# Optimization experiments

Hardware: AMD Instinct MI355X
Metric: run time of the kernel (lower is better)

The kernel has to match this reference:

```python
import jax, jax.numpy as jnp
import numpy as np

EPS = 1e-5
NEG = 0.1  # LeakyReLU slope


def _conv(x, w, stride=1, pad=0):
    return jax.lax.conv_general_dilated(
        x, w, (stride, stride), [(pad, pad), (pad, pad)],
        dimension_numbers=('NCHW', 'OIHW', 'NCHW'))


def _bn(x, p):
    # p: [4, C] stacked (gamma, beta, running_mean, running_var); eval-mode BN
    g, b, m, v = p[0], p[1], p[2], p[3]
    inv = g / jnp.sqrt(v + EPS)
    return x * inv[None, :, None, None] + (b - m * inv)[None, :, None, None]


def _lrelu(x):
    return jnp.where(x >= 0, x, NEG * x)


def _mdcn(x, w_off, b_off, w_dcn, b_dcn, G=2, K=3, pad=1):
    # ModulatedDeformConvPack (DCNv2): conv_offset -> (dy, dx, mask), then
    # modulated bilinear sampling + dense contraction with the conv weight.
    B, C, H, W = x.shape
    K2 = K * K
    off = _conv(x, w_off, 1, pad) + b_off[None, :, None, None]  # [B, 3*G*K2, H, W]
    dy, dx, ml = jnp.split(off, 3, axis=1)
    dy = dy.reshape(B, G, K2, H, W)
    dx = dx.reshape(B, G, K2, H, W)
    mask = jax.nn.sigmoid(ml).reshape(B, G, K2, H, W)
    kyv, kxv = np.meshgrid(np.arange(K), np.arange(K), indexing='ij')
    ky = jnp.asarray(kyv.reshape(K2), x.dtype)
    kx = jnp.asarray(kxv.reshape(K2), x.dtype)
    ii = jnp.arange(H, dtype=x.dtype)
    jj = jnp.arange(W, dtype=x.dtype)
    # sample coords: p0 + p_k + offset (stride 1, dilation 1)
    py = ii[None, None, None, :, None] - pad + ky[None, None, :, None, None] + dy
    px = jj[None, None, None, None, :] - pad + kx[None, None, :, None, None] + dx
    Cg = C // G
    # [B, G, H*W, Cg] layout so the bilinear gather indexes a small int tensor
    imgs = x.reshape(B, G, Cg, H, W).transpose(0, 1, 3, 4, 2).reshape(B, G, H * W, Cg)
    y0 = jnp.floor(py)
    x0 = jnp.floor(px)
    N = K2 * H * W
    wy = (py - y0).reshape(B, G, N, 1)
    wx = (px - x0).reshape(B, G, N, 1)

    def gather(yi, xi):
        valid = (yi >= 0) & (yi <= H - 1) & (xi >= 0) & (xi <= W - 1)
        yc = jnp.clip(yi, 0, H - 1).astype(jnp.int32)
        xc = jnp.clip(xi, 0, W - 1).astype(jnp.int32)
        idx = (yc * W + xc).reshape(B, G, N, 1)
        v = jnp.take_along_axis(imgs, idx, axis=2)  # [B, G, N, Cg]
        return v * valid.reshape(B, G, N, 1).astype(x.dtype)

    v00 = gather(y0, x0)
    v01 = gather(y0, x0 + 1)
    v10 = gather(y0 + 1, x0)
    v11 = gather(y0 + 1, x0 + 1)
    val = (v00 * (1 - wy) * (1 - wx) + v01 * (1 - wy) * wx
           + v10 * wy * (1 - wx) + v11 * wy * wx)
    val = (val * mask.reshape(B, G, N, 1)).reshape(B, G, K2, H, W, Cg)
    wr = w_dcn.reshape(w_dcn.shape[0], G, Cg, K2)
    out = jnp.einsum('bgkijc,ogck->boij', val, wr)
    return out + b_dcn[None, :, None, None]


def _forward(x, w_r1, bn_r1, w_r2, bn_r2, w_rs, bn_rs, w_off, b_off,
             w_dcn, b_dcn, bn1, w_c2, bn2, w_ds, bn_ds):
    # ResBlock(in=64, out=128, stride=2): conv3x3/s2-BN-LReLU-conv3x3-BN + 1x1/s2 shortcut
    h = _lrelu(_bn(_conv(x, w_r1, 2, 1), bn_r1))
    h = _bn(_conv(h, w_r2, 1, 1), bn_r2)
    sc = _bn(_conv(x, w_rs, 2, 0), bn_rs)
    h = _lrelu(h + sc)
    # modulated deformable conv 3x3, deformable_groups=2
    h = _lrelu(_bn(_mdcn(h, w_off, b_off, w_dcn, b_dcn), bn1))
    h = _lrelu(_bn(_conv(h, w_c2, 1, 0), bn2))
    # DeconBlock residual (downsample since in!=out, stride!=1)
    res = _bn(_conv(x, w_ds, 2, 0), bn_ds)
    return res + h


def setup_inputs() -> dict:
    key = jax.random.key(0)
    ks = jax.random.split(key, 16)
    f32 = jnp.float32

    def n(k, shape, s):
        return jax.random.normal(k, shape, f32) * s

    def bnp(k, c):
        # gamma, beta, mean, var — var kept >= 0.1 for stability
        return jax.random.uniform(k, (4, c), f32, 0.1, 1.0)

    return {
        'x': n(ks[0], (4, 64, 192, 192), 1.0),
        'w_r1': n(ks[1], (128, 64, 3, 3), 0.04),
        'bn_r1': bnp(ks[2], 128),
        'w_r2': n(ks[3], (128, 128, 3, 3), 0.03),
        'bn_r2': bnp(ks[4], 128),
        'w_rs': n(ks[5], (128, 64, 1, 1), 0.12),
        'bn_rs': bnp(ks[6], 128),
        'w_off': n(ks[7], (54, 128, 3, 3), 0.01),  # small => offsets of a few px
        'b_off': n(ks[8], (54,), 0.1),
        'w_dcn': n(ks[9], (128, 128, 3, 3), 0.03),
        'b_dcn': n(ks[10], (128,), 0.1),
        'bn1': bnp(ks[11], 128),
        'w_c2': n(ks[12], (128, 128, 1, 1), 0.09),
        'bn2': bnp(ks[13], 128),
        'w_ds': n(ks[14], (128, 64, 1, 1), 0.12),
        'bn_ds': bnp(ks[15], 128),
    }


def reference(x, w_r1, bn_r1, w_r2, bn_r2, w_rs, bn_rs, w_off, b_off,
              w_dcn, b_dcn, bn1, w_c2, bn2, w_ds, bn_ds):
    return _forward(x, w_r1, bn_r1, w_r2, bn_r2, w_rs, bn_rs, w_off, b_off,
                    w_dcn, b_dcn, bn1, w_c2, bn2, w_ds, bn_ds)
```

## Files before the change

### kernel.cpp

```cpp
#include <hip/hip_runtime.h>
#include <hip/hip_bf16.h>
#include <cstdint>

#define EPS 1e-5f
#define NEG 0.1f

using bfrag = __attribute__((ext_vector_type(8))) short;
using f32x4 = __attribute__((ext_vector_type(4))) float;
typedef unsigned short ushort_t;

constexpr int B_  = 4,  CIN = 64, H0 = 192, W0 = 192;
constexpr int C_  = 128, H_ = 96, W_ = 96;
constexpr int HW_ = H_ * W_;
constexpr int HW0 = H0 * W0;
constexpr int XS  = 194;
constexpr int TS  = 98;
constexpr int VSTR = 1160;

__device__ __forceinline__ ushort_t f2bf(float f) {
  unsigned u = __builtin_bit_cast(unsigned, f);
  u += 0x7fffu + ((u >> 16) & 1u);
  return (ushort_t)(u >> 16);
}
__device__ __forceinline__ float loF(unsigned d) {
  return __builtin_bit_cast(float, d << 16);
}
__device__ __forceinline__ float hiF(unsigned d) {
  return __builtin_bit_cast(float, d & 0xFFFF0000u);
}
__device__ __forceinline__ bfrag loadB(const ushort_t* p) {
  return *(const bfrag*)p;
}

#define MFMA4(A0, A1, B0, B1, ACC)                                             \
  ACC[0][0] = __builtin_amdgcn_mfma_f32_16x16x32_bf16(A0, B0, ACC[0][0], 0, 0, 0); \
  ACC[0][1] = __builtin_amdgcn_mfma_f32_16x16x32_bf16(A0, B1, ACC[0][1], 0, 0, 0); \
  ACC[1][0] = __builtin_amdgcn_mfma_f32_16x16x32_bf16(A1, B0, ACC[1][0], 0, 0, 0); \
  ACC[1][1] = __builtin_amdgcn_mfma_f32_16x16x32_bf16(A1, B1, ACC[1][1], 0, 0, 0);

__global__ __launch_bounds__(256)
void k_prep(const float* __restrict__ w_r1, const float* __restrict__ w_r2,
            const float* __restrict__ w_off, const float* __restrict__ w_dcn,
            const float* __restrict__ w_rs, const float* __restrict__ w_c2,
            const float* __restrict__ w_ds,
            ushort_t* __restrict__ wp_r1, ushort_t* __restrict__ wp_r2,
            ushort_t* __restrict__ wp_off, ushort_t* __restrict__ wp_dcn,
            ushort_t* __restrict__ wp_rs, ushort_t* __restrict__ wp_c2,
            ushort_t* __restrict__ wp_ds,
            ushort_t* __restrict__ xclp, ushort_t* __restrict__ t1p,
            ushort_t* __restrict__ t3p) {
  int bi = blockIdx.x;
  int tid = (int)threadIdx.x;
  auto pack3w = [&](const float* w, ushort_t* wp, int O, int C, int Opad, int b0) {
    int idx = (bi - b0) * 256 + tid;
    int e = idx & 7;
    int lane = (idx >> 3) & 63;
    int fb = idx >> 9;
    int OBQ = Opad / 16;
    int obq = fb % OBQ, s = fb / OBQ;
    int lr = lane & 15, lq = lane >> 4;
    int o = obq * 16 + lr;
    int cq = s % (C / 32), tap = s / (C / 32);
    int c = cq * 32 + lq * 8 + e;
    wp[idx] = (o < O) ? f2bf(w[((size_t)o * C + c) * 9 + tap]) : (ushort_t)0;
  };
  auto pack1w = [&](const float* w, ushort_t* wp, int O, int C, int Opad, int b0) {
    int idx = (bi - b0) * 256 + tid;
    int e = idx & 7;
    int lane = (idx >> 3) & 63;
    int fb = idx >> 9;
    int OBQ = Opad / 16;
    int obq = fb % OBQ, s = fb / OBQ;
    int lr = lane & 15, lq = lane >> 4;
    int o = obq * 16 + lr;
    int c = s * 32 + lq * 8 + e;
    wp[idx] = (o < O) ? f2bf(w[(size_t)o * C + c]) : (ushort_t)0;
  };
  auto border = [&](ushort_t* buf, int N, int C, int b0) {
    int idx = (bi - b0) * 256 + tid;
    int per = 4 * N - 4;
    if (idx >= per * 4) return;
    int b = idx / per, e = idx - b * per;
    int r, s;
    if (e < N) { r = 0; s = e; }
    else if (e < 2 * N) { r = N - 1; s = e - N; }
    else if (e < 3 * N - 2) { r = e - 2 * N + 1; s = 0; }
    else { r = e - (3 * N - 2) + 1; s = N - 1; }
    uint4* p = (uint4*)(buf + ((size_t)(b * N + r) * N + s) * C);
#pragma unroll
    for (int t = 0; t < 16; ++t) { if (t < C / 8) p[t] = make_uint4(0, 0, 0, 0); }
  };
  if      (bi <  288) pack3w(w_r1,  wp_r1, 128,  64, 128, 0);
  else if (bi <  864) pack3w(w_r2,  wp_r2, 128, 128, 128, 288);
  else if (bi < 1152) pack3w(w_off, wp_off, 54, 128,  64, 864);
  else if (bi < 1728) pack3w(w_dcn, wp_dcn, 128, 128, 128, 1152);
  else if (bi < 1760) pack1w(w_rs,  wp_rs, 128,  64, 128, 1728);
  else if (bi < 1824) pack1w(w_c2,  wp_c2, 128, 128, 128, 1760);
  else if (bi < 1856) pack1w(w_ds,  wp_ds, 128,  64, 128, 1824);
  else if (bi < 1869) border(xclp, XS, 64, 1856);
  else if (bi < 1876) border(t1p, TS, 128, 1869);
  else                border(t3p, TS, 128, 1876);
}

__global__ __launch_bounds__(256)
void k_xcl(const float* __restrict__ x, ushort_t* __restrict__ xclp) {
  __shared__ float tile[64][65];
  int tx = threadIdx.x, ty = threadIdx.y;
  int cx = blockIdx.x, y = blockIdx.y, b = blockIdx.z;
  const float* src = x + (size_t)b * CIN * HW0 + (size_t)y * W0 + cx * 64;
#pragma unroll
  for (int r = 0; r < 16; ++r) {
    int ch = r * 4 + ty;
    tile[ch][tx] = src[(size_t)ch * HW0 + tx];
  }
  __syncthreads();
  ushort_t* dst = xclp + ((size_t)(b * XS + y + 1) * XS + cx * 64 + 1) * 64;
#pragma unroll
  for (int r = 0; r < 16; ++r) {
    int pp = r * 4 + ty;
    dst[(size_t)pp * 64 + tx] = f2bf(tile[tx][pp]);
  }
}

__global__ __launch_bounds__(256)
void k_conv1(const ushort_t* __restrict__ xclp, const ushort_t* __restrict__ wp,
             const float* __restrict__ bnp, ushort_t* __restrict__ t1p) {
  __shared__ ushort_t at[3 * 66 * 64];
  int tid = threadIdx.x, lane = tid & 63, wv = tid >> 6;
  int lr = lane & 15, lq = lane >> 4, ob = wv * 32;
  int j0 = blockIdx.x * 32, i = blockIdx.y, b = blockIdx.z;
  for (int t = tid; t < 1584; t += 256) {
    int ky = t / 528, r = t - ky * 528;
    int p = r >> 3, c8 = r & 7;
    const char* src = (const char*)(xclp +
        ((size_t)(b * XS + 2 * i + ky) * XS + 2 * j0) * 64) + p * 128 + c8 * 16;
    int db = ((ky * 66 + p) * 128 + c8 * 16) ^ (((p >> 1) & 7) << 4);
    *(uint4*)((char*)at + db) = *(const uint4*)src;
  }
  __syncthreads();
  f32x4 acc[2][2] = {};
#pragma unroll
  for (int tap = 0; tap < 9; ++tap) {
    int ky = tap / 3, kx = tap - 3 * ky;
    int pxa = 2 * lr + kx, pxb = 2 * (16 + lr) + kx;
#pragma unroll
    for (int cq = 0; cq < 2; ++cq) {
      bfrag a0 = *(const bfrag*)((const char*)at +
          (((ky * 66 + pxa) * 128 + cq * 64 + lq * 16) ^ (((pxa >> 1) & 7) << 4)));
      bfrag a1 = *(const bfrag*)((const char*)at +
          (((ky * 66 + pxb) * 128 + cq * 64 + lq * 16) ^ (((pxb >> 1) & 7) << 4)));
      int s = tap * 2 + cq;
      bfrag b0 = loadB(wp + (size_t)(s * 8 + wv * 2) * 512 + lane * 8);
      bfrag b1 = loadB(wp + (size_t)(s * 8 + wv * 2 + 1) * 512 + lane * 8);
      MFMA4(a0, a1, b0, b1, acc);
    }
  }
  ushort_t* dst = t1p + ((size_t)(b * TS + i + 1) * TS + j0 + 1) * 128;
#pragma unroll
  for (int nf = 0; nf < 2; ++nf) {
    int o = ob + nf * 16 + lr;
    float inv = bnp[o] * rsqrtf(bnp[384 + o] + EPS);
    float bb = bnp[128 + o] - bnp[256 + o] * inv;
#pragma unroll
    for (int mf = 0; mf < 2; ++mf)
#pragma unroll
      for (int jj = 0; jj < 4; ++jj) {
        int pix = mf * 16 + 4 * lq + jj;
        float r = acc[mf][nf][jj] * inv + bb;
        r = r >= 0.f ? r : NEG * r;
        dst[(size_t)pix * 128 + o] = f2bf(r);
      }
  }
}

__global__ __launch_bounds__(256)
void k_conv2(const ushort_t* __restrict__ t1p, const ushort_t* __restrict__ xclp,
             const ushort_t* __restrict__ wp2, const ushort_t* __restrict__ wprs,
             const float* __restrict__ bn2p, const float* __restrict__ bnsp,
             ushort_t* __restrict__ t3p) {
  __shared__ ushort_t at[3 * 34 * 128];
  int tid = threadIdx.x, lane = tid & 63, wv = tid >> 6;
  int lr = lane & 15, lq = lane >> 4, ob = wv * 32;
  int j0 = blockIdx.x * 32, i = blockIdx.y, b = blockIdx.z;
  for (int t = tid; t < 1632; t += 256) {
    int ky = t / 544, r = t - ky * 544;
    int p = r >> 4, c16 = r & 15;
    const char* src = (const char*)(t1p +
        ((size_t)(b * TS + i + ky) * TS + j0) * 128) + p * 256 + c16 * 16;
    int db = ((ky * 34 + p) * 256 + c16 * 16) ^ ((p & 7) << 4);
    *(uint4*)((char*)at + db) = *(const uint4*)src;
  }
  __syncthreads();
  f32x4 acc[2][2] = {};
  f32x4 acs[2][2] = {};
#pragma unroll
  for (int tap = 0; tap < 9; ++tap) {
    int ky = tap / 3, kx = tap - 3 * ky;
    int pxa = lr + kx, pxb = 16 + lr + kx;
#pragma unroll
    for (int cq = 0; cq < 4; ++cq) {
      bfrag a0 = *(const bfrag*)((const char*)at +
          (((ky * 34 + pxa) * 256 + cq * 64 + lq * 16) ^ ((pxa & 7) << 4)));
      bfrag a1 = *(const bfrag*)((const char*)at +
          (((ky * 34 + pxb) * 256 + cq * 64 + lq * 16) ^ ((pxb & 7) << 4)));
      int s = tap * 4 + cq;
      bfrag b0 = loadB(wp2 + (size_t)(s * 8 + wv * 2) * 512 + lane * 8);
      bfrag b1 = loadB(wp2 + (size_t)(s * 8 + wv * 2 + 1) * 512 + lane * 8);
      MFMA4(a0, a1, b0, b1, acc);
    }
  }
  {
    const ushort_t* rowp = xclp + (size_t)(b * XS + 2 * i + 1) * XS * 64;
    const ushort_t* pa = rowp + (size_t)(2 * (j0 + lr) + 1) * 64 + 8 * lq;
    const ushort_t* pb = rowp + (size_t)(2 * (j0 + 16 + lr) + 1) * 64 + 8 * lq;
#pragma unroll
    for (int sq = 0; sq < 2; ++sq) {
      bfrag a0 = loadB(pa + sq * 32);
      bfrag a1 = loadB(pb + sq * 32);
      bfrag b0 = loadB(wprs + (size_t)(sq * 8 + wv * 2) * 512 + lane * 8);
      bfrag b1 = loadB(wprs + (size_t)(sq * 8 + wv * 2 + 1) * 512 + lane * 8);
      MFMA4(a0, a1, b0, b1, acs);
    }
  }
  ushort_t* dst = t3p + ((size_t)(b * TS + i + 1) * TS + j0 + 1) * 128;
#pragma unroll
  for (int nf = 0; nf < 2; ++nf) {
    int o = ob + nf * 16 + lr;
    float i2 = bn2p[o] * rsqrtf(bn2p[384 + o] + EPS);
    float b2 = bn2p[128 + o] - bn2p[256 + o] * i2;
    float is = bnsp[o] * rsqrtf(bnsp[384 + o] + EPS);
    float bs = bnsp[128 + o] - bnsp[256 + o] * is;
#pragma unroll
    for (int mf = 0; mf < 2; ++mf)
#pragma unroll
      for (int jj = 0; jj < 4; ++jj) {
        int pix = mf * 16 + 4 * lq + jj;
        float h = acc[mf][nf][jj] * i2 + b2 + acs[mf][nf][jj] * is + bs;
        h = h >= 0.f ? h : NEG * h;
        dst[(size_t)pix * 128 + o] = f2bf(h);
      }
  }
}

__global__ __launch_bounds__(128)
void k_convoff(const ushort_t* __restrict__ t3p, const ushort_t* __restrict__ wp,
               const float* __restrict__ boff, float* __restrict__ offb) {
  __shared__ ushort_t at[3 * 34 * 128];
  int tid = threadIdx.x, lane = tid & 63, wv = tid >> 6;
  int lr = lane & 15, lq = lane >> 4, ob = wv * 32;
  int j0 = blockIdx.x * 32, i = blockIdx.y, b = blockIdx.z;
  for (int t = tid; t < 1632; t += 128) {
    int ky = t / 544, r = t - ky * 544;
    int p = r >> 4, c16 = r & 15;
    const char* src = (const char*)(t3p +
        ((size_t)(b * TS + i + ky) * TS + j0) * 128) + p * 256 + c16 * 16;
    int db = ((ky * 34 + p) * 256 + c16 * 16) ^ ((p & 7) << 4);
    *(uint4*)((char*)at + db) = *(const uint4*)src;
  }
  __syncthreads();
  f32x4 acc[2][2] = {};
#pragma unroll
  for (int tap = 0; tap < 9; ++tap) {
    int ky = tap / 3, kx = tap - 3 * ky;
    int pxa = lr + kx, pxb = 16 + lr + kx;
#pragma unroll
    for (int cq = 0; cq < 4; ++cq) {
      bfrag a0 = *(const bfrag*)((const char*)at +
          (((ky * 34 + pxa) * 256 + cq * 64 + lq * 16) ^ ((pxa & 7) << 4)));
      bfrag a1 = *(const bfrag*)((const char*)at +
          (((ky * 34 + pxb) * 256 + cq * 64 + lq * 16) ^ ((pxb & 7) << 4)));
      int s = tap * 4 + cq;
      bfrag b0 = loadB(wp + (size_t)(s * 4 + wv * 2) * 512 + lane * 8);
      bfrag b1 = loadB(wp + (size_t)(s * 4 + wv * 2 + 1) * 512 + lane * 8);
      MFMA4(a0, a1, b0, b1, acc);
    }
  }
  float* dst = offb + ((size_t)b * HW_ + (size_t)i * W_ + j0) * 64;
#pragma unroll
  for (int nf = 0; nf < 2; ++nf) {
    int o = ob + nf * 16 + lr;
    float bias = (o < 54) ? boff[o] : 0.f;
#pragma unroll
    for (int mf = 0; mf < 2; ++mf)
#pragma unroll
      for (int jj = 0; jj < 4; ++jj) {
        int pix = mf * 16 + 4 * lq + jj;
        float v = (o < 54) ? acc[mf][nf][jj] + bias : 0.f;
        dst[(size_t)pix * 64 + o] = v;
      }
  }
}

__global__ __launch_bounds__(512)
void k_dcn(const ushort_t* __restrict__ t3p, const float* __restrict__ offb,
           const ushort_t* __restrict__ wp, const float* __restrict__ bdcn,
           const float* __restrict__ bnp, ushort_t* __restrict__ t4cl) {
  __shared__ ushort_t val[16 * VSTR];
  __shared__ int   pre_b[288];
  __shared__ uint2 pre_w[288];
  int tid = threadIdx.x;
  int j0 = blockIdx.x * 16, i = blockIdx.y, b = blockIdx.z;

  if (tid < 288) {
    int t = tid;
    int pix = t / 18, gk = t - pix * 18;
    int g = gk / 9, k = gk - 9 * g;
    int ky = k / 3, kx = k - 3 * ky;
    int j = j0 + pix;
    const float* ob_ = offb + ((size_t)b * HW_ + (size_t)i * W_ + j) * 64;
    float dy = ob_[gk];
    float dx = ob_[18 + gk];
    float ml = ob_[36 + gk];
    float mk = 1.f / (1.f + __expf(-ml));
    float py = (float)(i - 1 + ky) + dy;
    float px = (float)(j - 1 + kx) + dx;
    float fy = floorf(py), fx = floorf(px);
    float wy = py - fy, wx = px - fx;
    int y0 = (int)fy, x0 = (int)fx;
    bool yv0 = (unsigned)y0 < 96u, yv1 = (unsigned)(y0 + 1) < 96u;
    bool xv0 = (unsigned)x0 < 96u, xv1 = (unsigned)(x0 + 1) < 96u;
    float w00 = (yv0 && xv0) ? (1.f - wy) * (1.f - wx) * mk : 0.f;
    float w01 = (yv0 && xv1) ? (1.f - wy) * wx * mk : 0.f;
    float w10 = (yv1 && xv0) ? wy * (1.f - wx) * mk : 0.f;
    float w11 = (yv1 && xv1) ? wy * wx * mk : 0.f;
    int yb = min(max(y0, -1), 95), xb = min(max(x0, -1), 95);
    pre_b[t] = (((yb + 1) * TS + xb + 1) * 128 + g * 64) * 2;
    pre_w[t] = make_uint2((unsigned)f2bf(w00) | ((unsigned)f2bf(w01) << 16),
                          (unsigned)f2bf(w10) | ((unsigned)f2bf(w11) << 16));
  }
  __syncthreads();

  {
    int gq = tid >> 4;
    int c16 = tid & 15;
    int pix = gq >> 1, g = gq & 1;
    const char* imgb = (const char*)(t3p + (size_t)b * TS * TS * 128) + c16 * 8;
    int bidx = pix * 18 + g * 9;
    char* vrow = (char*)val + pix * (VSTR * 2) + g * 128 + c16 * 8;
#pragma unroll
    for (int k = 0; k < 9; ++k) {
      int gb = pre_b[bidx + k];
      uint2 ww = pre_w[bidx + k];
      const char* pA = imgb + gb;
      uint2 d00 = *(const uint2*)(pA);
      uint2 d01 = *(const uint2*)(pA + 256);
      uint2 d10 = *(const uint2*)(pA + TS * 256);
      uint2 d11 = *(const uint2*)(pA + TS * 256 + 256);
      float w00 = loF(ww.x), w01 = hiF(ww.x);
      float w10 = loF(ww.y), w11 = hiF(ww.y);
      unsigned o2[2];
#pragma unroll
      for (int t = 0; t < 2; ++t) {
        unsigned e00 = ((const unsigned*)&d00)[t];
        unsigned e01 = ((const unsigned*)&d01)[t];
        unsigned e10 = ((const unsigned*)&d10)[t];
        unsigned e11 = ((const unsigned*)&d11)[t];
        float slo = loF(e00) * w00 + loF(e01) * w01 + loF(e10) * w10 + loF(e11) * w11;
        float shi = hiF(e00) * w00 + hiF(e01) * w01 + hiF(e10) * w10 + hiF(e11) * w11;
        unsigned u0 = __builtin_bit_cast(unsigned, slo) + 0x8000u;
        unsigned u1 = __builtin_bit_cast(unsigned, shi) + 0x8000u;
        o2[t] = __builtin_amdgcn_perm(u1, u0, 0x07060302u);
      }
      *(uint2*)(vrow + k * 256) = make_uint2(o2[0], o2[1]);
    }
  }
  __syncthreads();

  int lane = tid & 63, wv = tid >> 6;
  int lr = lane & 15, lq = lane >> 4, ob = wv * 16;
  f32x4 acc = {};
  for (int s = 0; s < 36; ++s) {
    bfrag a0 = *(const bfrag*)&val[lr * VSTR + 32 * s + 8 * lq];
    bfrag b0 = loadB(wp + (size_t)(s * 8 + wv) * 512 + lane * 8);
    acc = __builtin_amdgcn_mfma_f32_16x16x32_bf16(a0, b0, acc, 0, 0, 0);
  }

  {
    ushort_t* dst = t4cl + ((size_t)(b * 96 + i) * 96 + j0) * 128;
    int o = ob + lr;
    float inv = bnp[o] * rsqrtf(bnp[384 + o] + EPS);
    float bb = bnp[128 + o] - bnp[256 + o] * inv;
    float bd = bdcn[o];
#pragma unroll
    for (int jj = 0; jj < 4; ++jj) {
      int pix = 4 * lq + jj;
      float r = (acc[jj] + bd) * inv + bb;
      r = r >= 0.f ? r : NEG * r;
      dst[(size_t)pix * 128 + o] = f2bf(r);
    }
  }
}

__global__ __launch_bounds__(256)
void k_final(const ushort_t* __restrict__ t4cl, const ushort_t* __restrict__ xclp,
             const ushort_t* __restrict__ wpc2, const ushort_t* __restrict__ wpds,
             const float* __restrict__ bn2p, const float* __restrict__ bndsp,
             float* __restrict__ outp) {
  __shared__ float ol[128 * 36];
  int tid = threadIdx.x, lane = tid & 63, wv = tid >> 6;
  int lr = lane & 15, lq = lane >> 4, ob = wv * 32;
  int j0 = blockIdx.x * 32, i = blockIdx.y, b = blockIdx.z;
  f32x4 acc[2][2] = {};
  f32x4 acs[2][2] = {};
  {
    const ushort_t* rowp = t4cl + ((size_t)(b * 96 + i) * 96 + j0) * 128;
#pragma unroll
    for (int s = 0; s < 4; ++s) {
      bfrag a0 = loadB(rowp + (size_t)lr * 128 + s * 32 + 8 * lq);
      bfrag a1 = loadB(rowp + (size_t)(16 + lr) * 128 + s * 32 + 8 * lq);
      bfrag b0 = loadB(wpc2 + (size_t)(s * 8 + wv * 2) * 512 + lane * 8);
      bfrag b1 = loadB(wpc2 + (size_t)(s * 8 + wv * 2 + 1) * 512 + lane * 8);
      MFMA4(a0, a1, b0, b1, acc);
    }
  }
  {
    const ushort_t* rowx = xclp + (size_t)(b * XS + 2 * i + 1) * XS * 64;
    const ushort_t* pa = rowx + (size_t)(2 * (j0 + lr) + 1) * 64 + 8 * lq;
    const ushort_t* pb = rowx + (size_t)(2 * (j0 + 16 + lr) + 1) * 64 + 8 * lq;
#pragma unroll
    for (int s = 0; s < 2; ++s) {
      bfrag a0 = loadB(pa + s * 32);
      bfrag a1 = loadB(pb + s * 32);
      bfrag b0 = loadB(wpds + (size_t)(s * 8 + wv * 2) * 512 + lane * 8);
      bfrag b1 = loadB(wpds + (size_t)(s * 8 + wv * 2 + 1) * 512 + lane * 8);
      MFMA4(a0, a1, b0, b1, acs);
    }
  }
#pragma unroll
  for (int nf = 0; nf < 2; ++nf) {
    int o = ob + nf * 16 + lr;
    float i2 = bn2p[o] * rsqrtf(bn2p[384 + o] + EPS);
    float b2 = bn2p[128 + o] - bn2p[256 + o] * i2;
    float id = bndsp[o] * rsqrtf(bndsp[384 + o] + EPS);
    float bd = bndsp[128 + o] - bndsp[256 + o] * id;
#pragma unroll
    for (int mf = 0; mf < 2; ++mf)
#pragma unroll
      for (int jj = 0; jj < 4; ++jj) {
        int pix = mf * 16 + 4 * lq + jj;
        float h = acc[mf][nf][jj] * i2 + b2;
        h = h >= 0.f ? h : NEG * h;
        float res = acs[mf][nf][jj] * id + bd;
        ol[o * 36 + pix] = res + h;
      }
  }
  __syncthreads();
#pragma unroll
  for (int r = 0; r < 4; ++r) {
    int idx = r * 256 + tid;
    int o = idx >> 3, p4 = idx & 7;
    f32x4 v = *(const f32x4*)&ol[o * 36 + p4 * 4];
    *(f32x4*)&outp[((size_t)(b * C_ + o) * H_ + i) * W_ + j0 + p4 * 4] = v;
  }
}

extern "C" void kernel_launch(void* const* d_in, const int* in_sizes, int n_in,
                              void* d_out, int out_size, void* d_ws, size_t ws_size,
                              hipStream_t stream) {
  const float* x     = (const float*)d_in[0];
  const float* w_r1  = (const float*)d_in[1];
  const float* bn_r1 = (const float*)d_in[2];
  const float* w_r2  = (const float*)d_in[3];
  const float* bn_r2 = (const float*)d_in[4];
  const float* w_rs  = (const float*)d_in[5];
  const float* bn_rs = (const float*)d_in[6];
  const float* w_off = (const float*)d_in[7];
  const float* b_off = (const float*)d_in[8];
  const float* w_dcn = (const float*)d_in[9];
  const float* b_dcn = (const float*)d_in[10];
  const float* bn1   = (const float*)d_in[11];
  const float* w_c2  = (const float*)d_in[12];
  const float* bn2   = (const float*)d_in[13];
  const float* w_ds  = (const float*)d_in[14];
  const float* bn_ds = (const float*)d_in[15];
  float* out = (float*)d_out;

  ushort_t* base  = (ushort_t*)d_ws;
  ushort_t* xclp  = base;
  ushort_t* t1p   = base + 9634816;
  ushort_t* t3p   = base + 14552064;
  ushort_t* wp_r1 = base + 19469312;
  ushort_t* wp_r2 = wp_r1 + 73728;
  ushort_t* wp_off= wp_r2 + 147456;
  ushort_t* wp_dcn= wp_off + 73728;
  ushort_t* wp_rs = wp_dcn + 147456;
  ushort_t* wp_c2 = wp_rs + 8192;
  ushort_t* wp_ds = wp_c2 + 16384;
  float*    offb  = (float*)t1p;
  ushort_t* t4cl  = t1p;

  k_prep<<<1883, 256, 0, stream>>>(w_r1, w_r2, w_off, w_dcn, w_rs, w_c2, w_ds,
                                   wp_r1, wp_r2, wp_off, wp_dcn, wp_rs, wp_c2,
                                   wp_ds, xclp, t1p, t3p);

  k_xcl    <<<dim3(3, 192, 4), dim3(64, 4), 0, stream>>>(x, xclp);
  k_conv1  <<<dim3(3, 96, 4), 256, 0, stream>>>(xclp, wp_r1, bn_r1, t1p);
  k_conv2  <<<dim3(3, 96, 4), 256, 0, stream>>>(t1p, xclp, wp_r2, wp_rs, bn_r2, bn_rs, t3p);
  k_convoff<<<dim3(3, 96, 4), 128, 0, stream>>>(t3p, wp_off, b_off, offb);
  k_dcn    <<<dim3(6, 96, 4), 512, 0, stream>>>(t3p, offb, wp_dcn, b_dcn, bn1, t4cl);
  k_final  <<<dim3(3, 96, 4), 256, 0, stream>>>(t4cl, xclp, wp_c2, wp_ds, bn2, bn_ds, out);
}
```

Before: 129.0 us.

## Split DCN contraction K across waves with LDS reduction

The deformable-conv GEMM stage previously gave each of the four waves 16 output channels, each looping over all 36 K-steps serially. Now each wave owns 64 output channels (4 MFMA tiles) and a quarter of the K range (9 steps). Partial sums go through LDS, where wave group 0 reduces them before the BN and LeakyReLU epilogue. This shortens the dependent MFMA chain and reuses each A fragment four times, at the cost of more accumulator registers, an extra barrier and an LDS reduction pass.

```diff
diff --git a/kernel.cpp b/kernel.cpp
--- a/kernel.cpp
+++ b/kernel.cpp
@@ -367,26 +367,52 @@
   __syncthreads();
 
   int lane = tid & 63, wv = tid >> 6;
-  int lr = lane & 15, lq = lane >> 4, ob = wv * 16;
-  f32x4 acc = {};
-  for (int s = 0; s < 36; ++s) {
+  int lr = lane & 15, lq = lane >> 4;
+  int wo = wv & 1, wk = wv >> 1;
+  f32x4 acc[4] = {};
+#pragma unroll
+  for (int s9 = 0; s9 < 9; ++s9) {
+    int s = wk * 9 + s9;
     bfrag a0 = *(const bfrag*)&val[lr * VSTR + 32 * s + 8 * lq];
-    bfrag b0 = loadB(wp + (size_t)(s * 8 + wv) * 512 + lane * 8);
-    acc = __builtin_amdgcn_mfma_f32_16x16x32_bf16(a0, b0, acc, 0, 0, 0);
-  }
-
-  {
+#pragma unroll
+    for (int ot = 0; ot < 4; ++ot) {
+      bfrag b0 = loadB(wp + (size_t)(s * 8 + wo * 4 + ot) * 512 + lane * 8);
+      acc[ot] = __builtin_amdgcn_mfma_f32_16x16x32_bf16(a0, b0, acc[ot], 0, 0, 0);
+    }
+  }
+  __syncthreads();
+  float* red = (float*)val;
+  if (wk > 0) {
+    float* dst = red + (size_t)((wk - 1) * 2 + wo) * 1024 + lane * 4;
+#pragma unroll
+    for (int ot = 0; ot < 4; ++ot)
+      *(f32x4*)(dst + ot * 256) = acc[ot];
+  }
+  __syncthreads();
+  if (wk == 0) {
+#pragma unroll
+    for (int w = 0; w < 3; ++w) {
+      const float* src = red + (size_t)(w * 2 + wo) * 1024 + lane * 4;
+#pragma unroll
+      for (int ot = 0; ot < 4; ++ot) {
+        f32x4 v = *(const f32x4*)(src + ot * 256);
+        acc[ot] += v;
+      }
+    }
     ushort_t* dst = t4cl + ((size_t)(b * 96 + i) * 96 + j0) * 128;
-    int o = ob + lr;
-    float inv = bnp[o] * rsqrtf(bnp[384 + o] + EPS);
-    float bb = bnp[128 + o] - bnp[256 + o] * inv;
-    float bd = bdcn[o];
-#pragma unroll
-    for (int jj = 0; jj < 4; ++jj) {
-      int pix = 4 * lq + jj;
-      float r = (acc[jj] + bd) * inv + bb;
-      r = r >= 0.f ? r : NEG * r;
-      dst[(size_t)pix * 128 + o] = f2bf(r);
+#pragma unroll
+    for (int ot = 0; ot < 4; ++ot) {
+      int o = wo * 64 + ot * 16 + lr;
+      float inv = bnp[o] * rsqrtf(bnp[384 + o] + EPS);
+      float bb = bnp[128 + o] - bnp[256 + o] * inv;
+      float bd = bdcn[o];
+#pragma unroll
+      for (int jj = 0; jj < 4; ++jj) {
+        int pix = 4 * lq + jj;
+        float r = (acc[ot][jj] + bd) * inv + bb;
+        r = r >= 0.f ? r : NEG * r;
+        dst[(size_t)pix * 128 + o] = f2bf(r);
+      }
     }
   }
 }
```

Result: no change. 129.4 us (+0.3%).

## Compute DCN sampling params per lane, broadcast via shuffles, and prefetch taps

Applied to the files above, without the earlier changes.

The deformable conv kernel no longer computes offset, mask and bilinear weights in 288 threads into shared memory followed by a block barrier. Each 16-lane group now computes its own 9 taps in lanes 0-8 and broadcasts them with wave shuffles. The gather loop is software-pipelined: the four corner loads for the next tap are issued before the current tap is blended, with a sched_barrier to keep that order. This removes one __syncthreads and the shared-memory round trip, and hides gather latency, at the cost of more registers, shuffle instructions and redundant lanes 9-15 sitting idle during setup.

```diff
diff --git a/kernel.cpp b/kernel.cpp
--- a/kernel.cpp
+++ b/kernel.cpp
@@ -296,15 +296,17 @@
            const ushort_t* __restrict__ wp, const float* __restrict__ bdcn,
            const float* __restrict__ bnp, ushort_t* __restrict__ t4cl) {
   __shared__ ushort_t val[16 * VSTR];
-  __shared__ int   pre_b[288];
-  __shared__ uint2 pre_w[288];
   int tid = threadIdx.x;
   int j0 = blockIdx.x * 16, i = blockIdx.y, b = blockIdx.z;
-
-  if (tid < 288) {
-    int t = tid;
-    int pix = t / 18, gk = t - pix * 18;
-    int g = gk / 9, k = gk - 9 * g;
+  int lane = tid & 63, wv = tid >> 6;
+  int gq = tid >> 4;
+  int c16 = tid & 15;
+  int pix = gq >> 1, g = gq & 1;
+  int gl = (gq & 3) * 16;
+
+  int my_b = 0; unsigned my_w0 = 0, my_w1 = 0;
+  if (c16 < 9) {
+    int k = c16, gk = g * 9 + k;
     int ky = k / 3, kx = k - 3 * ky;
     int j = j0 + pix;
     const float* ob_ = offb + ((size_t)b * HW_ + (size_t)i * W_ + j) * 64;
@@ -324,49 +326,58 @@
     float w10 = (yv1 && xv0) ? wy * (1.f - wx) * mk : 0.f;
     float w11 = (yv1 && xv1) ? wy * wx * mk : 0.f;
     int yb = min(max(y0, -1), 95), xb = min(max(x0, -1), 95);
-    pre_b[t] = (((yb + 1) * TS + xb + 1) * 128 + g * 64) * 2;
-    pre_w[t] = make_uint2((unsigned)f2bf(w00) | ((unsigned)f2bf(w01) << 16),
-                          (unsigned)f2bf(w10) | ((unsigned)f2bf(w11) << 16));
+    my_b = (((yb + 1) * TS + xb + 1) * 128 + g * 64) * 2;
+    my_w0 = (unsigned)f2bf(w00) | ((unsigned)f2bf(w01) << 16);
+    my_w1 = (unsigned)f2bf(w10) | ((unsigned)f2bf(w11) << 16);
+  }
+
+  const char* imgb = (const char*)(t3p + (size_t)b * TS * TS * 128) + c16 * 8;
+  char* vrow = (char*)val + pix * (VSTR * 2) + g * 128 + c16 * 8;
+
+  int gb_c = __shfl(my_b, gl + 0, 64);
+  unsigned w0_c = (unsigned)__shfl((int)my_w0, gl + 0, 64);
+  unsigned w1_c = (unsigned)__shfl((int)my_w1, gl + 0, 64);
+  const char* pC = imgb + gb_c;
+  uint2 d00 = *(const uint2*)pC;
+  uint2 d01 = *(const uint2*)(pC + 256);
+  uint2 d10 = *(const uint2*)(pC + TS * 256);
+  uint2 d11 = *(const uint2*)(pC + TS * 256 + 256);
+#pragma unroll
+  for (int k = 0; k < 9; ++k) {
+    uint2 n00 = {}, n01 = {}, n10 = {}, n11 = {};
+    unsigned w0_n = 0, w1_n = 0;
+    if (k < 8) {
+      int gb_n = __shfl(my_b, gl + k + 1, 64);
+      w0_n = (unsigned)__shfl((int)my_w0, gl + k + 1, 64);
+      w1_n = (unsigned)__shfl((int)my_w1, gl + k + 1, 64);
+      const char* pN = imgb + gb_n;
+      n00 = *(const uint2*)pN;
+      n01 = *(const uint2*)(pN + 256);
+      n10 = *(const uint2*)(pN + TS * 256);
+      n11 = *(const uint2*)(pN + TS * 256 + 256);
+    }
+    __builtin_amdgcn_sched_barrier(0);
+    float w00 = loF(w0_c), w01 = hiF(w0_c);
+    float w10 = loF(w1_c), w11 = hiF(w1_c);
+    unsigned o2[2];
+#pragma unroll
+    for (int t = 0; t < 2; ++t) {
+      unsigned e00 = ((const unsigned*)&d00)[t];
+      unsigned e01 = ((const unsigned*)&d01)[t];
+      unsigned e10 = ((const unsigned*)&d10)[t];
+      unsigned e11 = ((const unsigned*)&d11)[t];
+      float slo = loF(e00) * w00 + loF(e01) * w01 + loF(e10) * w10 + loF(e11) * w11;
+      float shi = hiF(e00) * w00 + hiF(e01) * w01 + hiF(e10) * w10 + hiF(e11) * w11;
+      unsigned u0 = __builtin_bit_cast(unsigned, slo) + 0x8000u;
+      unsigned u1 = __builtin_bit_cast(unsigned, shi) + 0x8000u;
+      o2[t] = __builtin_amdgcn_perm(u1, u0, 0x07060302u);
+    }
+    *(uint2*)(vrow + k * 256) = make_uint2(o2[0], o2[1]);
+    d00 = n00; d01 = n01; d10 = n10; d11 = n11;
+    w0_c = w0_n; w1_c = w1_n;
   }
   __syncthreads();
 
-  {
-    int gq = tid >> 4;
-    int c16 = tid & 15;
-    int pix = gq >> 1, g = gq & 1;
-    const char* imgb = (const char*)(t3p + (size_t)b * TS * TS * 128) + c16 * 8;
-    int bidx = pix * 18 + g * 9;
-    char* vrow = (char*)val + pix * (VSTR * 2) + g * 128 + c16 * 8;
-#pragma unroll
-    for (int k = 0; k < 9; ++k) {
-      int gb = pre_b[bidx + k];
-      uint2 ww = pre_w[bidx + k];
-      const char* pA = imgb + gb;
-      uint2 d00 = *(const uint2*)(pA);
-      uint2 d01 = *(const uint2*)(pA + 256);
-      uint2 d10 = *(const uint2*)(pA + TS * 256);
-      uint2 d11 = *(const uint2*)(pA + TS * 256 + 256);
-      float w00 = loF(ww.x), w01 = hiF(ww.x);
-      float w10 = loF(ww.y), w11 = hiF(ww.y);
-      unsigned o2[2];
-#pragma unroll
-      for (int t = 0; t < 2; ++t) {
-        unsigned e00 = ((const unsigned*)&d00)[t];
-        unsigned e01 = ((const unsigned*)&d01)[t];
-        unsigned e10 = ((const unsigned*)&d10)[t];
-        unsigned e11 = ((const unsigned*)&d11)[t];
-        float slo = loF(e00) * w00 + loF(e01) * w01 + loF(e10) * w10 + loF(e11) * w11;
-        float shi = hiF(e00) * w00 + hiF(e01) * w01 + hiF(e10) * w10 + hiF(e11) * w11;
-        unsigned u0 = __builtin_bit_cast(unsigned, slo) + 0x8000u;
-        unsigned u1 = __builtin_bit_cast(unsigned, shi) + 0x8000u;
-        o2[t] = __builtin_amdgcn_perm(u1, u0, 0x07060302u);
-      }
-      *(uint2*)(vrow + k * 256) = make_uint2(o2[0], o2[1]);
-    }
-  }
-  __syncthreads();
-
-  int lane = tid & 63, wv = tid >> 6;
   int lr = lane & 15, lq = lane >> 4, ob = wv * 16;
   f32x4 acc = {};
   for (int s = 0; s < 36; ++s) {
@@ -383,10 +394,10 @@
     float bd = bdcn[o];
 #pragma unroll
     for (int jj = 0; jj < 4; ++jj) {
-      int pix = 4 * lq + jj;
+      int pixw = 4 * lq + jj;
       float r = (acc[jj] + bd) * inv + bb;
       r = r >= 0.f ? r : NEG * r;
-      dst[(size_t)pix * 128 + o] = f2bf(r);
+      dst[(size_t)pixw * 128 + o] = f2bf(r);
     }
   }
 }
```

Result: no change. 127.7 us (-1.0%).

## Compute two output rows per block in convs and 32 pixels per DCN block

Applied to the files above, without the earlier changes.

conv1 and conv2 now give each block two output rows. The halo rows are shared in LDS, and each weight fragment loaded from global memory feeds twice as many MFMAs. The grid is halved along y. The DCN kernel now covers 32 pixels per block, with 512 threads each handling one pixel. Sampling offsets and bilinear weights are computed in registers and broadcast with warp shuffles instead of going through LDS precompute arrays. This trades more registers and LDS per block, and fewer blocks, for less weight traffic and fewer barriers.

```diff
diff --git a/kernel.cpp b/kernel.cpp
--- a/kernel.cpp
+++ b/kernel.cpp
@@ -125,51 +125,58 @@
 __global__ __launch_bounds__(256)
 void k_conv1(const ushort_t* __restrict__ xclp, const ushort_t* __restrict__ wp,
              const float* __restrict__ bnp, ushort_t* __restrict__ t1p) {
-  __shared__ ushort_t at[3 * 66 * 64];
+  __shared__ ushort_t at[5 * 66 * 64];
   int tid = threadIdx.x, lane = tid & 63, wv = tid >> 6;
   int lr = lane & 15, lq = lane >> 4, ob = wv * 32;
-  int j0 = blockIdx.x * 32, i = blockIdx.y, b = blockIdx.z;
-  for (int t = tid; t < 1584; t += 256) {
+  int j0 = blockIdx.x * 32, i0 = blockIdx.y * 2, b = blockIdx.z;
+  for (int t = tid; t < 2640; t += 256) {
     int ky = t / 528, r = t - ky * 528;
     int p = r >> 3, c8 = r & 7;
     const char* src = (const char*)(xclp +
-        ((size_t)(b * XS + 2 * i + ky) * XS + 2 * j0) * 64) + p * 128 + c8 * 16;
+        ((size_t)(b * XS + 2 * i0 + ky) * XS + 2 * j0) * 64) + p * 128 + c8 * 16;
     int db = ((ky * 66 + p) * 128 + c8 * 16) ^ (((p >> 1) & 7) << 4);
     *(uint4*)((char*)at + db) = *(const uint4*)src;
   }
   __syncthreads();
-  f32x4 acc[2][2] = {};
+  f32x4 acc[2][2][2] = {};
 #pragma unroll
   for (int tap = 0; tap < 9; ++tap) {
     int ky = tap / 3, kx = tap - 3 * ky;
     int pxa = 2 * lr + kx, pxb = 2 * (16 + lr) + kx;
 #pragma unroll
     for (int cq = 0; cq < 2; ++cq) {
-      bfrag a0 = *(const bfrag*)((const char*)at +
-          (((ky * 66 + pxa) * 128 + cq * 64 + lq * 16) ^ (((pxa >> 1) & 7) << 4)));
-      bfrag a1 = *(const bfrag*)((const char*)at +
-          (((ky * 66 + pxb) * 128 + cq * 64 + lq * 16) ^ (((pxb >> 1) & 7) << 4)));
       int s = tap * 2 + cq;
       bfrag b0 = loadB(wp + (size_t)(s * 8 + wv * 2) * 512 + lane * 8);
       bfrag b1 = loadB(wp + (size_t)(s * 8 + wv * 2 + 1) * 512 + lane * 8);
-      MFMA4(a0, a1, b0, b1, acc);
-    }
-  }
-  ushort_t* dst = t1p + ((size_t)(b * TS + i + 1) * TS + j0 + 1) * 128;
-#pragma unroll
-  for (int nf = 0; nf < 2; ++nf) {
-    int o = ob + nf * 16 + lr;
-    float inv = bnp[o] * rsqrtf(bnp[384 + o] + EPS);
-    float bb = bnp[128 + o] - bnp[256 + o] * inv;
-#pragma unroll
-    for (int mf = 0; mf < 2; ++mf)
-#pragma unroll
-      for (int jj = 0; jj < 4; ++jj) {
-        int pix = mf * 16 + 4 * lq + jj;
-        float r = acc[mf][nf][jj] * inv + bb;
-        r = r >= 0.f ? r : NEG * r;
-        dst[(size_t)pix * 128 + o] = f2bf(r);
+#pragma unroll
+      for (int r = 0; r < 2; ++r) {
+        int kr = 2 * r + ky;
+        bfrag a0 = *(const bfrag*)((const char*)at +
+            (((kr * 66 + pxa) * 128 + cq * 64 + lq * 16) ^ (((pxa >> 1) & 7) << 4)));
+        bfrag a1 = *(const bfrag*)((const char*)at +
+            (((kr * 66 + pxb) * 128 + cq * 64 + lq * 16) ^ (((pxb >> 1) & 7) << 4)));
+        MFMA4(a0, a1, b0, b1, acc[r]);
       }
+    }
+  }
+#pragma unroll
+  for (int r = 0; r < 2; ++r) {
+    ushort_t* dst = t1p + ((size_t)(b * TS + i0 + r + 1) * TS + j0 + 1) * 128;
+#pragma unroll
+    for (int nf = 0; nf < 2; ++nf) {
+      int o = ob + nf * 16 + lr;
+      float inv = bnp[o] * rsqrtf(bnp[384 + o] + EPS);
+      float bb = bnp[128 + o] - bnp[256 + o] * inv;
+#pragma unroll
+      for (int mf = 0; mf < 2; ++mf)
+#pragma unroll
+        for (int jj = 0; jj < 4; ++jj) {
+          int pix = mf * 16 + 4 * lq + jj;
+          float v = acc[r][mf][nf][jj] * inv + bb;
+          v = v >= 0.f ? v : NEG * v;
+          dst[(size_t)pix * 128 + o] = f2bf(v);
+        }
+    }
   }
 }
 
@@ -178,39 +185,44 @@
              const ushort_t* __restrict__ wp2, const ushort_t* __restrict__ wprs,
              const float* __restrict__ bn2p, const float* __restrict__ bnsp,
              ushort_t* __restrict__ t3p) {
-  __shared__ ushort_t at[3 * 34 * 128];
+  __shared__ ushort_t at[4 * 34 * 128];
   int tid = threadIdx.x, lane = tid & 63, wv = tid >> 6;
   int lr = lane & 15, lq = lane >> 4, ob = wv * 32;
-  int j0 = blockIdx.x * 32, i = blockIdx.y, b = blockIdx.z;
-  for (int t = tid; t < 1632; t += 256) {
+  int j0 = blockIdx.x * 32, i0 = blockIdx.y * 2, b = blockIdx.z;
+  for (int t = tid; t < 2176; t += 256) {
     int ky = t / 544, r = t - ky * 544;
     int p = r >> 4, c16 = r & 15;
     const char* src = (const char*)(t1p +
-        ((size_t)(b * TS + i + ky) * TS + j0) * 128) + p * 256 + c16 * 16;
+        ((size_t)(b * TS + i0 + ky) * TS + j0) * 128) + p * 256 + c16 * 16;
     int db = ((ky * 34 + p) * 256 + c16 * 16) ^ ((p & 7) << 4);
     *(uint4*)((char*)at + db) = *(const uint4*)src;
   }
   __syncthreads();
-  f32x4 acc[2][2] = {};
-  f32x4 acs[2][2] = {};
+  f32x4 acc[2][2][2] = {};
+  f32x4 acs[2][2][2] = {};
 #pragma unroll
   for (int tap = 0; tap < 9; ++tap) {
     int ky = tap / 3, kx = tap - 3 * ky;
     int pxa = lr + kx, pxb = 16 + lr + kx;
 #pragma unroll
     for (int cq = 0; cq < 4; ++cq) {
-      bfrag a0 = *(const bfrag*)((const char*)at +
-          (((ky * 34 + pxa) * 256 + cq * 64 + lq * 16) ^ ((pxa & 7) << 4)));
-      bfrag a1 = *(const bfrag*)((const char*)at +
-          (((ky * 34 + pxb) * 256 + cq * 64 + lq * 16) ^ ((pxb & 7) << 4)));
       int s = tap * 4 + cq;
       bfrag b0 = loadB(wp2 + (size_t)(s * 8 + wv * 2) * 512 + lane * 8);
       bfrag b1 = loadB(wp2 + (size_t)(s * 8 + wv * 2 + 1) * 512 + lane * 8);
-      MFMA4(a0, a1, b0, b1, acc);
-    }
-  }
-  {
-    const ushort_t* rowp = xclp + (size_t)(b * XS + 2 * i + 1) * XS * 64;
+#pragma unroll
+      for (int r = 0; r < 2; ++r) {
+        int kr = r + ky;
+        bfrag a0 = *(const bfrag*)((const char*)at +
+            (((kr * 34 + pxa) * 256 + cq * 64 + lq * 16) ^ ((pxa & 7) << 4)));
+        bfrag a1 = *(const bfrag*)((const char*)at +
+            (((kr * 34 + pxb) * 256 + cq * 64 + lq * 16) ^ ((pxb & 7) << 4)));
+        MFMA4(a0, a1, b0, b1, acc[r]);
+      }
+    }
+  }
+#pragma unroll
+  for (int r = 0; r < 2; ++r) {
+    const ushort_t* rowp = xclp + (size_t)(b * XS + 2 * (i0 + r) + 1) * XS * 64;
     const ushort_t* pa = rowp + (size_t)(2 * (j0 + lr) + 1) * 64 + 8 * lq;
     const ushort_t* pb = rowp + (size_t)(2 * (j0 + 16 + lr) + 1) * 64 + 8 * lq;
 #pragma unroll
@@ -219,26 +231,29 @@
       bfrag a1 = loadB(pb + sq * 32);
       bfrag b0 = loadB(wprs + (size_t)(sq * 8 + wv * 2) * 512 + lane * 8);
       bfrag b1 = loadB(wprs + (size_t)(sq * 8 + wv * 2 + 1) * 512 + lane * 8);
-      MFMA4(a0, a1, b0, b1, acs);
-    }
-  }
-  ushort_t* dst = t3p + ((size_t)(b * TS + i + 1) * TS + j0 + 1) * 128;
-#pragma unroll
-  for (int nf = 0; nf < 2; ++nf) {
-    int o = ob + nf * 16 + lr;
-    float i2 = bn2p[o] * rsqrtf(bn2p[384 + o] + EPS);
-    float b2 = bn2p[128 + o] - bn2p[256 + o] * i2;
-    float is = bnsp[o] * rsqrtf(bnsp[384 + o] + EPS);
-    float bs = bnsp[128 + o] - bnsp[256 + o] * is;
-#pragma unroll
-    for (int mf = 0; mf < 2; ++mf)
-#pragma unroll
-      for (int jj = 0; jj < 4; ++jj) {
-        int pix = mf * 16 + 4 * lq + jj;
-        float h = acc[mf][nf][jj] * i2 + b2 + acs[mf][nf][jj] * is + bs;
-        h = h >= 0.f ? h : NEG * h;
-        dst[(size_t)pix * 128 + o] = f2bf(h);
-      }
+      MFMA4(a0, a1, b0, b1, acs[r]);
+    }
+  }
+#pragma unroll
+  for (int r = 0; r < 2; ++r) {
+    ushort_t* dst = t3p + ((size_t)(b * TS + i0 + r + 1) * TS + j0 + 1) * 128;
+#pragma unroll
+    for (int nf = 0; nf < 2; ++nf) {
+      int o = ob + nf * 16 + lr;
+      float i2 = bn2p[o] * rsqrtf(bn2p[384 + o] + EPS);
+      float b2 = bn2p[128 + o] - bn2p[256 + o] * i2;
+      float is = bnsp[o] * rsqrtf(bnsp[384 + o] + EPS);
+      float bs = bnsp[128 + o] - bnsp[256 + o] * is;
+#pragma unroll
+      for (int mf = 0; mf < 2; ++mf)
+#pragma unroll
+        for (int jj = 0; jj < 4; ++jj) {
+          int pix = mf * 16 + 4 * lq + jj;
+          float h = acc[r][mf][nf][jj] * i2 + b2 + acs[r][mf][nf][jj] * is + bs;
+          h = h >= 0.f ? h : NEG * h;
+          dst[(size_t)pix * 128 + o] = f2bf(h);
+        }
+    }
   }
 }
 
@@ -295,59 +310,65 @@
 void k_dcn(const ushort_t* __restrict__ t3p, const float* __restrict__ offb,
            const ushort_t* __restrict__ wp, const float* __restrict__ bdcn,
            const float* __restrict__ bnp, ushort_t* __restrict__ t4cl) {
-  __shared__ ushort_t val[16 * VSTR];
-  __shared__ int   pre_b[288];
-  __shared__ uint2 pre_w[288];
+  __shared__ ushort_t val[32 * VSTR];
   int tid = threadIdx.x;
-  int j0 = blockIdx.x * 16, i = blockIdx.y, b = blockIdx.z;
-
-  if (tid < 288) {
-    int t = tid;
-    int pix = t / 18, gk = t - pix * 18;
-    int g = gk / 9, k = gk - 9 * g;
+  int j0 = blockIdx.x * 32, i = blockIdx.y, b = blockIdx.z;
+  int lane = tid & 63, wv = tid >> 6;
+  int gq = tid >> 4;
+  int c16 = tid & 15;
+  int gl = (gq & 3) * 16;
+
+  int my_b0 = 0, my_b1 = 0;
+  unsigned my_w00 = 0, my_w10 = 0, my_w01 = 0, my_w11 = 0;
+  if (c16 < 9) {
+    int k = c16;
     int ky = k / 3, kx = k - 3 * ky;
-    int j = j0 + pix;
+    int j = j0 + gq;
     const float* ob_ = offb + ((size_t)b * HW_ + (size_t)i * W_ + j) * 64;
-    float dy = ob_[gk];
-    float dx = ob_[18 + gk];
-    float ml = ob_[36 + gk];
-    float mk = 1.f / (1.f + __expf(-ml));
-    float py = (float)(i - 1 + ky) + dy;
-    float px = (float)(j - 1 + kx) + dx;
-    float fy = floorf(py), fx = floorf(px);
-    float wy = py - fy, wx = px - fx;
-    int y0 = (int)fy, x0 = (int)fx;
-    bool yv0 = (unsigned)y0 < 96u, yv1 = (unsigned)(y0 + 1) < 96u;
-    bool xv0 = (unsigned)x0 < 96u, xv1 = (unsigned)(x0 + 1) < 96u;
-    float w00 = (yv0 && xv0) ? (1.f - wy) * (1.f - wx) * mk : 0.f;
-    float w01 = (yv0 && xv1) ? (1.f - wy) * wx * mk : 0.f;
-    float w10 = (yv1 && xv0) ? wy * (1.f - wx) * mk : 0.f;
-    float w11 = (yv1 && xv1) ? wy * wx * mk : 0.f;
-    int yb = min(max(y0, -1), 95), xb = min(max(x0, -1), 95);
-    pre_b[t] = (((yb + 1) * TS + xb + 1) * 128 + g * 64) * 2;
-    pre_w[t] = make_uint2((unsigned)f2bf(w00) | ((unsigned)f2bf(w01) << 16),
-                          (unsigned)f2bf(w10) | ((unsigned)f2bf(w11) << 16));
-  }
-  __syncthreads();
-
-  {
-    int gq = tid >> 4;
-    int c16 = tid & 15;
-    int pix = gq >> 1, g = gq & 1;
-    const char* imgb = (const char*)(t3p + (size_t)b * TS * TS * 128) + c16 * 8;
-    int bidx = pix * 18 + g * 9;
-    char* vrow = (char*)val + pix * (VSTR * 2) + g * 128 + c16 * 8;
+#pragma unroll
+    for (int g = 0; g < 2; ++g) {
+      int gk = g * 9 + k;
+      float dy = ob_[gk];
+      float dx = ob_[18 + gk];
+      float ml = ob_[36 + gk];
+      float mk = 1.f / (1.f + __expf(-ml));
+      float py = (float)(i - 1 + ky) + dy;
+      float px = (float)(j - 1 + kx) + dx;
+      float fy = floorf(py), fx = floorf(px);
+      float wy = py - fy, wx = px - fx;
+      int y0 = (int)fy, x0 = (int)fx;
+      bool yv0 = (unsigned)y0 < 96u, yv1 = (unsigned)(y0 + 1) < 96u;
+      bool xv0 = (unsigned)x0 < 96u, xv1 = (unsigned)(x0 + 1) < 96u;
+      float w00 = (yv0 && xv0) ? (1.f - wy) * (1.f - wx) * mk : 0.f;
+      float w01 = (yv0 && xv1) ? (1.f - wy) * wx * mk : 0.f;
+      float w10 = (yv1 && xv0) ? wy * (1.f - wx) * mk : 0.f;
+      float w11 = (yv1 && xv1) ? wy * wx * mk : 0.f;
+      int yb = min(max(y0, -1), 95), xb = min(max(x0, -1), 95);
+      int bb = (((yb + 1) * TS + xb + 1) * 128 + g * 64) * 2;
+      unsigned pw0 = (unsigned)f2bf(w00) | ((unsigned)f2bf(w01) << 16);
+      unsigned pw1 = (unsigned)f2bf(w10) | ((unsigned)f2bf(w11) << 16);
+      if (g == 0) { my_b0 = bb; my_w00 = pw0; my_w10 = pw1; }
+      else        { my_b1 = bb; my_w01 = pw0; my_w11 = pw1; }
+    }
+  }
+
+  const char* imgb = (const char*)(t3p + (size_t)b * TS * TS * 128) + c16 * 8;
+  char* vrow = (char*)val + gq * (VSTR * 2) + c16 * 8;
+
+#pragma unroll
+  for (int g = 0; g < 2; ++g) {
 #pragma unroll
     for (int k = 0; k < 9; ++k) {
-      int gb = pre_b[bidx + k];
-      uint2 ww = pre_w[bidx + k];
+      int gb = __shfl(g == 0 ? my_b0 : my_b1, gl + k, 64);
+      unsigned w0 = (unsigned)__shfl((int)(g == 0 ? my_w00 : my_w01), gl + k, 64);
+      unsigned w1 = (unsigned)__shfl((int)(g == 0 ? my_w10 : my_w11), gl + k, 64);
       const char* pA = imgb + gb;
-      uint2 d00 = *(const uint2*)(pA);
+      uint2 d00 = *(const uint2*)pA;
       uint2 d01 = *(const uint2*)(pA + 256);
       uint2 d10 = *(const uint2*)(pA + TS * 256);
       uint2 d11 = *(const uint2*)(pA + TS * 256 + 256);
-      float w00 = loF(ww.x), w01 = hiF(ww.x);
-      float w10 = loF(ww.y), w11 = hiF(ww.y);
+      float w00 = loF(w0), w01 = hiF(w0);
+      float w10 = loF(w1), w11 = hiF(w1);
       unsigned o2[2];
 #pragma unroll
       for (int t = 0; t < 2; ++t) {
@@ -361,18 +382,19 @@
         unsigned u1 = __builtin_bit_cast(unsigned, shi) + 0x8000u;
         o2[t] = __builtin_amdgcn_perm(u1, u0, 0x07060302u);
       }
-      *(uint2*)(vrow + k * 256) = make_uint2(o2[0], o2[1]);
+      *(uint2*)(vrow + k * 256 + g * 128) = make_uint2(o2[0], o2[1]);
     }
   }
   __syncthreads();
 
-  int lane = tid & 63, wv = tid >> 6;
   int lr = lane & 15, lq = lane >> 4, ob = wv * 16;
-  f32x4 acc = {};
+  f32x4 acc0 = {}, acc1 = {};
   for (int s = 0; s < 36; ++s) {
     bfrag a0 = *(const bfrag*)&val[lr * VSTR + 32 * s + 8 * lq];
+    bfrag a1 = *(const bfrag*)&val[(16 + lr) * VSTR + 32 * s + 8 * lq];
     bfrag b0 = loadB(wp + (size_t)(s * 8 + wv) * 512 + lane * 8);
-    acc = __builtin_amdgcn_mfma_f32_16x16x32_bf16(a0, b0, acc, 0, 0, 0);
+    acc0 = __builtin_amdgcn_mfma_f32_16x16x32_bf16(a0, b0, acc0, 0, 0, 0);
+    acc1 = __builtin_amdgcn_mfma_f32_16x16x32_bf16(a1, b0, acc1, 0, 0, 0);
   }
 
   {
@@ -383,10 +405,13 @@
     float bd = bdcn[o];
 #pragma unroll
     for (int jj = 0; jj < 4; ++jj) {
-      int pix = 4 * lq + jj;
-      float r = (acc[jj] + bd) * inv + bb;
-      r = r >= 0.f ? r : NEG * r;
-      dst[(size_t)pix * 128 + o] = f2bf(r);
+      int p0 = 4 * lq + jj;
+      float r0 = (acc0[jj] + bd) * inv + bb;
+      r0 = r0 >= 0.f ? r0 : NEG * r0;
+      dst[(size_t)p0 * 128 + o] = f2bf(r0);
+      float r1 = (acc1[jj] + bd) * inv + bb;
+      r1 = r1 >= 0.f ? r1 : NEG * r1;
+      dst[(size_t)(16 + p0) * 128 + o] = f2bf(r1);
     }
   }
 }
@@ -494,9 +519,9 @@
                                    wp_ds, xclp, t1p, t3p);
 
   k_xcl    <<<dim3(3, 192, 4), dim3(64, 4), 0, stream>>>(x, xclp);
-  k_conv1  <<<dim3(3, 96, 4), 256, 0, stream>>>(xclp, wp_r1, bn_r1, t1p);
-  k_conv2  <<<dim3(3, 96, 4), 256, 0, stream>>>(t1p, xclp, wp_r2, wp_rs, bn_r2, bn_rs, t3p);
+  k_conv1  <<<dim3(3, 48, 4), 256, 0, stream>>>(xclp, wp_r1, bn_r1, t1p);
+  k_conv2  <<<dim3(3, 48, 4), 256, 0, stream>>>(t1p, xclp, wp_r2, wp_rs, bn_r2, bn_rs, t3p);
   k_convoff<<<dim3(3, 96, 4), 128, 0, stream>>>(t3p, wp_off, b_off, offb);
-  k_dcn    <<<dim3(6, 96, 4), 512, 0, stream>>>(t3p, offb, wp_dcn, b_dcn, bn1, t4cl);
+  k_dcn    <<<dim3(3, 96, 4), 512, 0, stream>>>(t3p, offb, wp_dcn, b_dcn, bn1, t4cl);
   k_final  <<<dim3(3, 96, 4), 256, 0, stream>>>(t4cl, xclp, wp_c2, wp_ds, bn2, bn_ds, out);
 }
```

Measured after the change: 128.1 us. No clear change (-0.7%).
